# Optimization experiments

Measured on AMD Instinct MI355X. Metric: run time of the kernel, lower is better.

Reference implementation:

```python
import jax, jax.numpy as jnp
import numpy as np

NUM_TAGS = 64
START_TAG = 62
STOP_TAG = 63
NEG = -10000.0
B, L = 512, 512


def setup_inputs() -> dict:
    key = jax.random.key(0)
    k1, k2, k3 = jax.random.split(key, 3)
    inputs = jax.random.normal(k1, (B, L, NUM_TAGS), dtype=jnp.float32)
    tags = jax.random.randint(k2, (B, L), 0, 62)  # real tags only (exclude sentinels)
    mask = jnp.ones((B, L), dtype=jnp.int32)
    transitions = jax.random.normal(k3, (NUM_TAGS, NUM_TAGS), dtype=jnp.float32)
    # match torch __init__: transitions[start_tag, :] = -10000; transitions[:, stop_tag] = -10000
    transitions = transitions.at[START_TAG, :].set(NEG).at[:, STOP_TAG].set(NEG)
    return {"inputs": inputs, "tags": tags, "mask": mask, "transitions": transitions}


def crf_loss(inputs, transitions, tags, mask):
    # inputs: [B, L, T] emissions; transitions[next, prev]; tags/mask: [B, L]
    Bb, Ll, T = inputs.shape
    maskf = mask.astype(inputs.dtype)

    # ---- denominator: forward algorithm (log-sum-exp recurrence over time) ----
    init_alphas = jnp.full((Bb, T), NEG, dtype=inputs.dtype).at[:, START_TAG].set(0.0)

    def step(forward_var, xs):
        emit, m = xs  # emit: [B, T], m: [B]
        # scores[b, next, prev] = fv[b, prev] + (transitions[next, prev] + emit[b, next]) * m[b]
        scores = forward_var[:, None, :] + (transitions[None, :, :] + emit[:, :, None]) * m[:, None, None]
        return jax.nn.logsumexp(scores, axis=-1), None

    forward_var, _ = jax.lax.scan(step, init_alphas, (jnp.swapaxes(inputs, 0, 1), maskf.T))
    terminal = forward_var + transitions[STOP_TAG][None, :]
    log_denominator = jax.nn.logsumexp(terminal, axis=-1)  # [B]

    # ---- numerator: score of the gold tag sequence (fully vectorized over time) ----
    score = transitions[tags[:, 0], START_TAG]  # [B]
    prev_t, next_t = tags[:, :-1], tags[:, 1:]
    trans_sc = transitions[next_t, prev_t]  # [B, L-1]
    emit_sc = jnp.take_along_axis(inputs[:, :-1, :], prev_t[:, :, None], axis=2)[..., 0]  # [B, L-1]
    score = score + jnp.sum(trans_sc * maskf[:, 1:] + emit_sc * maskf[:, :-1], axis=1)
    last_emit = jnp.take_along_axis(inputs[:, -1, :], tags[:, -1:], axis=1)[:, 0]
    score = score + transitions[STOP_TAG, tags[:, -1]] + last_emit * maskf[:, -1]

    return jnp.sum(score - log_denominator)


def reference(inputs, tags, mask, transitions):
    return crf_loss(inputs, transitions, tags, mask)
```

## Files before the change

kernel.cpp:

```cpp
#include <hip/hip_runtime.h>

namespace {

typedef float v2f __attribute__((ext_vector_type(2)));

constexpr int NTAGS = 64;
constexpr int START_T = 62;
constexpr int STOP_T = 63;
constexpr float NEGV = -10000.0f;
constexpr int Bc = 512;
constexpr int Lc = 512;

__device__ __forceinline__ float rfl_f(float v) {
  return __int_as_float(__builtin_amdgcn_readfirstlane(__float_as_int(v)));
}

__device__ __forceinline__ float wave_max(float v) {
#pragma unroll
  for (int off = 32; off >= 1; off >>= 1)
    v = fmaxf(v, __shfl_xor(v, off, 64));
  return v;
}

__device__ __forceinline__ float wave_sum(float v) {
#pragma unroll
  for (int off = 32; off >= 1; off >>= 1)
    v += __shfl_xor(v, off, 64);
  return v;
}

__global__ __launch_bounds__(64, 1) void crf_scan(
    const float* __restrict__ inputs,
    const int* __restrict__ tags,
    const int* __restrict__ mask,
    const float* __restrict__ trans,
    float* __restrict__ partial) {
  __shared__ float4 u4[16];
  float* u1 = reinterpret_cast<float*>(u4);

  const int b = blockIdx.x;
  const int lane = threadIdx.x;

#define FOR16(X) X(0) X(1) X(2) X(3) X(4) X(5) X(6) X(7) \
                 X(8) X(9) X(10) X(11) X(12) X(13) X(14) X(15)

#define DECL_E(q) v2f Ea##q, Eb##q;
  FOR16(DECL_E)
  {
    const float4* row = reinterpret_cast<const float4*>(trans + lane * NTAGS);
#define LOAD_E(q)                                     \
    {                                                 \
      float4 t = row[q];                              \
      Ea##q = (v2f){__expf(t.x), __expf(t.y)};        \
      Eb##q = (v2f){__expf(t.z), __expf(t.w)};        \
    }
    FOR16(LOAD_E)
  }

  const float* emit_base = inputs + (size_t)b * Lc * NTAGS;
  const float* pe = emit_base + lane;
  const int* mask_b = mask + b * Lc;
  const int* tags_b = tags + b * Lc;

  float alpha = (lane == START_T) ? 0.0f : NEGV;
  float m = 0.0f;

#define MF(q, A, B)                                   \
    {                                                 \
      float4 uu = u4[q];                              \
      A += Ea##q * (v2f){uu.x, uu.y};                 \
      B += Eb##q * (v2f){uu.z, uu.w};                 \
    }
#define MS(q)                                         \
    {                                                 \
      float4 uu = u4[q];                              \
      a0 += (v2f){uu.x, uu.y};                        \
      a1 += (v2f){uu.z, uu.w};                        \
    }

#define STEP(EMIT, MIDX)                                              \
    {                                                                 \
      float u_ = __expf(alpha - m);                                   \
      u1[lane] = u_;                                                  \
      __builtin_amdgcn_wave_barrier();                                \
      int mv = __builtin_amdgcn_readlane(mrow, (MIDX));               \
      if (mv) {                                                       \
        v2f a0 = {0.f, 0.f}, a1 = {0.f, 0.f};                         \
        v2f a2 = {0.f, 0.f}, a3 = {0.f, 0.f};                         \
        MF(0, a0, a1) MF(1, a2, a3) MF(2, a0, a1) MF(3, a2, a3)       \
        MF(4, a0, a1) MF(5, a2, a3) MF(6, a0, a1) MF(7, a2, a3)       \
        MF(8, a0, a1) MF(9, a2, a3) MF(10, a0, a1) MF(11, a2, a3)     \
        MF(12, a0, a1) MF(13, a2, a3) MF(14, a0, a1) MF(15, a2, a3)   \
        v2f t = (a0 + a1) + (a2 + a3);                                \
        alpha = __logf(t.x + t.y) + m + (EMIT);                       \
      } else {                                                        \
        v2f a0 = {0.f, 0.f}, a1 = {0.f, 0.f};                         \
        MS(0) MS(1) MS(2) MS(3) MS(4) MS(5) MS(6) MS(7)               \
        MS(8) MS(9) MS(10) MS(11) MS(12) MS(13) MS(14) MS(15)         \
        v2f t = a0 + a1;                                              \
        alpha = __logf(t.x + t.y) + m;                                \
      }                                                               \
      __builtin_amdgcn_wave_barrier();                                \
      m = rfl_f(alpha);                                               \
    }

#define PRE(B0, B1, B2, B3, ST)                                       \
    {                                                                 \
      int s_ = (ST); s_ = s_ > (Lc - 4) ? (Lc - 4) : s_;              \
      B0 = pe[(size_t)(s_ + 0) * NTAGS];                              \
      B1 = pe[(size_t)(s_ + 1) * NTAGS];                              \
      B2 = pe[(size_t)(s_ + 2) * NTAGS];                              \
      B3 = pe[(size_t)(s_ + 3) * NTAGS];                              \
    }

  float eA0, eA1, eA2, eA3, eB0, eB1, eB2, eB3;
  PRE(eA0, eA1, eA2, eA3, 0)
  int mrow = mask_b[lane];

  for (int chunk = 0; chunk < 8; ++chunk) {
    const int cbase = chunk * 64;
    int mrow_nxt = mask_b[(chunk < 7 ? cbase + 64 : cbase) + lane];
    for (int gp = 0; gp < 8; ++gp) {
      const int base = cbase + gp * 8;
      const int mb = gp * 8;
      PRE(eB0, eB1, eB2, eB3, base + 4)
      STEP(eA0, mb + 0) STEP(eA1, mb + 1) STEP(eA2, mb + 2) STEP(eA3, mb + 3)
      PRE(eA0, eA1, eA2, eA3, base + 8)
      STEP(eB0, mb + 4) STEP(eB1, mb + 5) STEP(eB2, mb + 6) STEP(eB3, mb + 7)
    }
    mrow = mrow_nxt;
  }

  float term = alpha + trans[STOP_T * NTAGS + lane];
  float mx = wave_max(term);
  float sden = wave_sum(__expf(term - mx));
  float logden = mx + __logf(sden);

  float sc = 0.0f;
  for (int l = lane; l < Lc; l += 64) {
    int tl = tags_b[l];
    float mfl = (float)mask_b[l];
    if (l < Lc - 1) {
      int tn = tags_b[l + 1];
      float mfn = (float)mask_b[l + 1];
      sc += trans[tn * NTAGS + tl] * mfn +
            emit_base[(size_t)l * NTAGS + tl] * mfl;
    } else {
      sc += trans[STOP_T * NTAGS + tl] +
            emit_base[(size_t)l * NTAGS + tl] * mfl;
    }
  }
  if (lane == 0) sc += trans[tags_b[0] * NTAGS + START_T];
  float score = wave_sum(sc);

  if (lane == 0) partial[b] = score - logden;
}

__global__ void crf_reduce(const float* __restrict__ partial,
                           float* __restrict__ out) {
  const int lane = threadIdx.x;
  float s = 0.0f;
  for (int i = lane; i < Bc; i += 64) s += partial[i];
  s = wave_sum(s);
  if (lane == 0) out[0] = s;
}

}

extern "C" void kernel_launch(void* const* d_in, const int* in_sizes, int n_in,
                              void* d_out, int out_size, void* d_ws,
                              size_t ws_size, hipStream_t stream) {
  const float* inputs = (const float*)d_in[0];
  const int* tags = (const int*)d_in[1];
  const int* mask = (const int*)d_in[2];
  const float* trans = (const float*)d_in[3];
  float* out = (float*)d_out;
  float* partial = (float*)d_ws;

  crf_scan<<<Bc, 64, 0, stream>>>(inputs, tags, mask, trans, partial);
  crf_reduce<<<1, 64, 0, stream>>>(partial, out);
}
```

Baseline: 162.1 us.

## Run CRF forward recurrence in linear space with power-of-two rescaling

Replaces the log-domain forward recurrence with a linear-domain one. Emissions are pre-exponentiated when loaded, and the per-step log/exp pair is removed. Each step rescales the state by a power of two taken from lane 0's exponent bits and keeps a running integer exponent sum, so ln2 is applied only once at the end. This shortens the serial dependency chain per time step, but it risks underflow or overflow when tags differ widely from lane 0 in magnitude.

```diff
diff --git a/kernel.cpp b/kernel.cpp
--- a/kernel.cpp
+++ b/kernel.cpp
@@ -7,13 +7,8 @@
 constexpr int NTAGS = 64;
 constexpr int START_T = 62;
 constexpr int STOP_T = 63;
-constexpr float NEGV = -10000.0f;
 constexpr int Bc = 512;
 constexpr int Lc = 512;
-
-__device__ __forceinline__ float rfl_f(float v) {
-  return __int_as_float(__builtin_amdgcn_readfirstlane(__float_as_int(v)));
-}
 
 __device__ __forceinline__ float wave_max(float v) {
 #pragma unroll
@@ -35,8 +30,8 @@
     const int* __restrict__ mask,
     const float* __restrict__ trans,
     float* __restrict__ partial) {
-  __shared__ float4 u4[16];
-  float* u1 = reinterpret_cast<float*>(u4);
+  __shared__ float4 vb4[16];
+  float* vb1 = reinterpret_cast<float*>(vb4);
 
   const int b = blockIdx.x;
   const int lane = threadIdx.x;
@@ -62,28 +57,27 @@
   const int* mask_b = mask + b * Lc;
   const int* tags_b = tags + b * Lc;
 
-  float alpha = (lane == START_T) ? 0.0f : NEGV;
-  float m = 0.0f;
+  int Msum = 0;
+  vb1[lane] = (lane == START_T) ? 1.0f : 0.0f;
+  __builtin_amdgcn_wave_barrier();
 
-#define MF(q, A, B)                                   \
+#define MF(q, A, Bq)                                  \
     {                                                 \
-      float4 uu = u4[q];                              \
+      float4 uu = vb4[q];                             \
       A += Ea##q * (v2f){uu.x, uu.y};                 \
-      B += Eb##q * (v2f){uu.z, uu.w};                 \
+      Bq += Eb##q * (v2f){uu.z, uu.w};                \
     }
 #define MS(q)                                         \
     {                                                 \
-      float4 uu = u4[q];                              \
+      float4 uu = vb4[q];                             \
       a0 += (v2f){uu.x, uu.y};                        \
       a1 += (v2f){uu.z, uu.w};                        \
     }
 
-#define STEP(EMIT, MIDX)                                              \
+#define STEP(W, MIDX)                                                 \
     {                                                                 \
-      float u_ = __expf(alpha - m);                                   \
-      u1[lane] = u_;                                                  \
-      __builtin_amdgcn_wave_barrier();                                \
-      int mv = __builtin_amdgcn_readlane(mrow, (MIDX));               \
+      const int mv = __builtin_amdgcn_readlane(mrow, (MIDX));         \
+      float s;                                                        \
       if (mv) {                                                       \
         v2f a0 = {0.f, 0.f}, a1 = {0.f, 0.f};                         \
         v2f a2 = {0.f, 0.f}, a3 = {0.f, 0.f};                         \
@@ -92,25 +86,32 @@
         MF(8, a0, a1) MF(9, a2, a3) MF(10, a0, a1) MF(11, a2, a3)     \
         MF(12, a0, a1) MF(13, a2, a3) MF(14, a0, a1) MF(15, a2, a3)   \
         v2f t = (a0 + a1) + (a2 + a3);                                \
-        alpha = __logf(t.x + t.y) + m + (EMIT);                       \
+        s = (t.x + t.y) * (W);                                        \
       } else {                                                        \
         v2f a0 = {0.f, 0.f}, a1 = {0.f, 0.f};                         \
         MS(0) MS(1) MS(2) MS(3) MS(4) MS(5) MS(6) MS(7)               \
         MS(8) MS(9) MS(10) MS(11) MS(12) MS(13) MS(14) MS(15)         \
         v2f t = a0 + a1;                                              \
-        alpha = __logf(t.x + t.y) + m;                                \
+        s = t.x + t.y;                                                \
       }                                                               \
+      const unsigned sb =                                             \
+          (unsigned)__builtin_amdgcn_readfirstlane(__float_as_int(s));\
+      const unsigned e0 = (sb >> 23) & 0xffu;                         \
+      Msum += (int)e0 - 127;                                          \
+      const float r = __uint_as_float((254u - e0) << 23);             \
+      const float vv = s * r;                                         \
       __builtin_amdgcn_wave_barrier();                                \
-      m = rfl_f(alpha);                                               \
+      vb1[lane] = vv;                                                 \
+      __builtin_amdgcn_wave_barrier();                                \
     }
 
 #define PRE(B0, B1, B2, B3, ST)                                       \
     {                                                                 \
       int s_ = (ST); s_ = s_ > (Lc - 4) ? (Lc - 4) : s_;              \
-      B0 = pe[(size_t)(s_ + 0) * NTAGS];                              \
-      B1 = pe[(size_t)(s_ + 1) * NTAGS];                              \
-      B2 = pe[(size_t)(s_ + 2) * NTAGS];                              \
-      B3 = pe[(size_t)(s_ + 3) * NTAGS];                              \
+      B0 = __expf(pe[(size_t)(s_ + 0) * NTAGS]);                      \
+      B1 = __expf(pe[(size_t)(s_ + 1) * NTAGS]);                      \
+      B2 = __expf(pe[(size_t)(s_ + 2) * NTAGS]);                      \
+      B3 = __expf(pe[(size_t)(s_ + 3) * NTAGS]);                      \
     }
 
   float eA0, eA1, eA2, eA3, eB0, eB1, eB2, eB3;
@@ -131,7 +132,11 @@
     mrow = mrow_nxt;
   }
 
-  float term = alpha + trans[STOP_T * NTAGS + lane];
+  const float mf = (float)Msum;
+  const float C = fmaf(mf, -2.1219444e-4f, mf * 0.693359375f);
+
+  float alphav = __logf(vb1[lane]) + C;
+  float term = alphav + trans[STOP_T * NTAGS + lane];
   float mx = wave_max(term);
   float sden = wave_sum(__expf(term - mx));
   float logden = mx + __logf(sden);
```

Result: faster. 152.1 us (-6.2%).

## Interleave two batch rows per wave and scan in linear domain with exponent rescaling

Applied to the files above, without the earlier changes.

Each wave now processes two sequences, alternating their recurrence steps so one chain's LDS round trip and math can overlap the other's. The per-step exp/log of the log-sum-exp is replaced by a linear-domain recurrence. Emissions are exponentiated on prefetch, and scaling uses a power-of-two factor taken from lane 0's float exponent, with the total shift tracked as an integer and converted to log only at the end. Only 256 blocks launch, which halves wave count on a 256-CU part, and the power-of-two rescaling risks underflow or precision loss if values spread widely.

```diff
diff --git a/kernel.cpp b/kernel.cpp
--- a/kernel.cpp
+++ b/kernel.cpp
@@ -7,13 +7,8 @@
 constexpr int NTAGS = 64;
 constexpr int START_T = 62;
 constexpr int STOP_T = 63;
-constexpr float NEGV = -10000.0f;
 constexpr int Bc = 512;
 constexpr int Lc = 512;
-
-__device__ __forceinline__ float rfl_f(float v) {
-  return __int_as_float(__builtin_amdgcn_readfirstlane(__float_as_int(v)));
-}
 
 __device__ __forceinline__ float wave_max(float v) {
 #pragma unroll
@@ -35,11 +30,14 @@
     const int* __restrict__ mask,
     const float* __restrict__ trans,
     float* __restrict__ partial) {
-  __shared__ float4 u4[16];
-  float* u1 = reinterpret_cast<float*>(u4);
-
-  const int b = blockIdx.x;
+  __shared__ float4 bufA[16];
+  __shared__ float4 bufB[16];
+  float* bA1 = reinterpret_cast<float*>(bufA);
+  float* bB1 = reinterpret_cast<float*>(bufB);
+
   const int lane = threadIdx.x;
+  const int bA = blockIdx.x;
+  const int bB = blockIdx.x + 256;
 
 #define FOR16(X) X(0) X(1) X(2) X(3) X(4) X(5) X(6) X(7) \
                  X(8) X(9) X(10) X(11) X(12) X(13) X(14) X(15)
@@ -57,103 +55,155 @@
     FOR16(LOAD_E)
   }
 
-  const float* emit_base = inputs + (size_t)b * Lc * NTAGS;
-  const float* pe = emit_base + lane;
-  const int* mask_b = mask + b * Lc;
-  const int* tags_b = tags + b * Lc;
-
-  float alpha = (lane == START_T) ? 0.0f : NEGV;
-  float m = 0.0f;
-
-#define MF(q, A, B)                                   \
+  const float* embA = inputs + (size_t)bA * Lc * NTAGS;
+  const float* embB = inputs + (size_t)bB * Lc * NTAGS;
+  const float* emA = embA + lane;
+  const float* emB = embB + lane;
+  const int* mAp = mask + bA * Lc;
+  const int* mBp = mask + bB * Lc;
+
+  int MsA = 0, MsB = 0;
+  bA1[lane] = (lane == START_T) ? 1.0f : 0.0f;
+  bB1[lane] = (lane == START_T) ? 1.0f : 0.0f;
+  __builtin_amdgcn_wave_barrier();
+
+  float4 uA[16], uB[16];
+#define ULOAD(U, BUF)                                  \
+  { _Pragma("unroll") for (int q_ = 0; q_ < 16; ++q_) U[q_] = BUF[q_]; }
+
+#define MF(U, q, A, B)                                \
     {                                                 \
-      float4 uu = u4[q];                              \
+      float4 uu = U[q];                               \
       A += Ea##q * (v2f){uu.x, uu.y};                 \
       B += Eb##q * (v2f){uu.z, uu.w};                 \
     }
-#define MS(q)                                         \
+#define MSUM(U, q, A, B)                              \
     {                                                 \
-      float4 uu = u4[q];                              \
-      a0 += (v2f){uu.x, uu.y};                        \
-      a1 += (v2f){uu.z, uu.w};                        \
-    }
-
-#define STEP(EMIT, MIDX)                                              \
-    {                                                                 \
-      float u_ = __expf(alpha - m);                                   \
-      u1[lane] = u_;                                                  \
-      __builtin_amdgcn_wave_barrier();                                \
-      int mv = __builtin_amdgcn_readlane(mrow, (MIDX));               \
-      if (mv) {                                                       \
-        v2f a0 = {0.f, 0.f}, a1 = {0.f, 0.f};                         \
-        v2f a2 = {0.f, 0.f}, a3 = {0.f, 0.f};                         \
-        MF(0, a0, a1) MF(1, a2, a3) MF(2, a0, a1) MF(3, a2, a3)       \
-        MF(4, a0, a1) MF(5, a2, a3) MF(6, a0, a1) MF(7, a2, a3)       \
-        MF(8, a0, a1) MF(9, a2, a3) MF(10, a0, a1) MF(11, a2, a3)     \
-        MF(12, a0, a1) MF(13, a2, a3) MF(14, a0, a1) MF(15, a2, a3)   \
-        v2f t = (a0 + a1) + (a2 + a3);                                \
-        alpha = __logf(t.x + t.y) + m + (EMIT);                       \
-      } else {                                                        \
-        v2f a0 = {0.f, 0.f}, a1 = {0.f, 0.f};                         \
-        MS(0) MS(1) MS(2) MS(3) MS(4) MS(5) MS(6) MS(7)               \
-        MS(8) MS(9) MS(10) MS(11) MS(12) MS(13) MS(14) MS(15)         \
-        v2f t = a0 + a1;                                              \
-        alpha = __logf(t.x + t.y) + m;                                \
-      }                                                               \
-      __builtin_amdgcn_wave_barrier();                                \
-      m = rfl_f(alpha);                                               \
-    }
-
-#define PRE(B0, B1, B2, B3, ST)                                       \
-    {                                                                 \
-      int s_ = (ST); s_ = s_ > (Lc - 4) ? (Lc - 4) : s_;              \
-      B0 = pe[(size_t)(s_ + 0) * NTAGS];                              \
-      B1 = pe[(size_t)(s_ + 1) * NTAGS];                              \
-      B2 = pe[(size_t)(s_ + 2) * NTAGS];                              \
-      B3 = pe[(size_t)(s_ + 3) * NTAGS];                              \
-    }
-
-  float eA0, eA1, eA2, eA3, eB0, eB1, eB2, eB3;
-  PRE(eA0, eA1, eA2, eA3, 0)
-  int mrow = mask_b[lane];
+      float4 uu = U[q];                               \
+      A += (v2f){uu.x, uu.y};                         \
+      B += (v2f){uu.z, uu.w};                         \
+    }
+
+#define COMPUTE(U, W, MROW, MIDX, MS, SOUT)                                 \
+    float SOUT;                                                             \
+    {                                                                       \
+      const int sb_ =                                                       \
+          __builtin_amdgcn_readfirstlane(__float_as_int(U[0].x));           \
+      const unsigned e0_ = ((unsigned)sb_ >> 23) & 0xffu;                   \
+      const int d_ = (e0_ == 0u) ? 0 : (int)e0_ - 127;                      \
+      MS += d_;                                                             \
+      const float rs_ = __uint_as_float((unsigned)(127 - d_) << 23);        \
+      const int mv_ = __builtin_amdgcn_readlane(MROW, (MIDX));              \
+      if (mv_) {                                                            \
+        v2f a0 = {0.f, 0.f}, a1 = {0.f, 0.f};                               \
+        v2f a2 = {0.f, 0.f}, a3 = {0.f, 0.f};                               \
+        MF(U, 0, a0, a1) MF(U, 1, a2, a3) MF(U, 2, a0, a1)                  \
+        MF(U, 3, a2, a3) MF(U, 4, a0, a1) MF(U, 5, a2, a3)                  \
+        MF(U, 6, a0, a1) MF(U, 7, a2, a3) MF(U, 8, a0, a1)                  \
+        MF(U, 9, a2, a3) MF(U, 10, a0, a1) MF(U, 11, a2, a3)                \
+        MF(U, 12, a0, a1) MF(U, 13, a2, a3) MF(U, 14, a0, a1)               \
+        MF(U, 15, a2, a3)                                                   \
+        v2f t_ = (a0 + a1) + (a2 + a3);                                     \
+        SOUT = (t_.x + t_.y) * ((W) * rs_);                                 \
+      } else {                                                              \
+        v2f a0 = {0.f, 0.f}, a1 = {0.f, 0.f};                               \
+        MSUM(U, 0, a0, a1) MSUM(U, 1, a0, a1) MSUM(U, 2, a0, a1)            \
+        MSUM(U, 3, a0, a1) MSUM(U, 4, a0, a1) MSUM(U, 5, a0, a1)            \
+        MSUM(U, 6, a0, a1) MSUM(U, 7, a0, a1) MSUM(U, 8, a0, a1)            \
+        MSUM(U, 9, a0, a1) MSUM(U, 10, a0, a1) MSUM(U, 11, a0, a1)          \
+        MSUM(U, 12, a0, a1) MSUM(U, 13, a0, a1) MSUM(U, 14, a0, a1)         \
+        MSUM(U, 15, a0, a1)                                                 \
+        v2f t_ = a0 + a1;                                                   \
+        SOUT = (t_.x + t_.y) * rs_;                                         \
+      }                                                                     \
+    }
+
+#define ITER(WA_, WB_, MIDX)                           \
+  {                                                    \
+    COMPUTE(uA, WA_, mrA, MIDX, MsA, sA_)              \
+    __builtin_amdgcn_wave_barrier();                   \
+    bA1[lane] = sA_;                                   \
+    __builtin_amdgcn_wave_barrier();                   \
+    ULOAD(uA, bufA)                                    \
+    COMPUTE(uB, WB_, mrB, MIDX, MsB, sB_)              \
+    __builtin_amdgcn_wave_barrier();                   \
+    bB1[lane] = sB_;                                   \
+    __builtin_amdgcn_wave_barrier();                   \
+    ULOAD(uB, bufB)                                    \
+  }
+
+#define PRE(Wb, EM, ST)                                                \
+  {                                                                    \
+    int s_ = (ST); s_ = s_ > (Lc - 4) ? (Lc - 4) : s_;                 \
+    _Pragma("unroll") for (int q_ = 0; q_ < 4; ++q_)                   \
+        Wb[q_] = __expf(EM[(size_t)(s_ + q_) * NTAGS]);                \
+  }
+
+  float wA0[4], wA1v[4], wB0[4], wB1v[4];
+  PRE(wA0, emA, 0)
+  PRE(wB0, emB, 0)
+  int mrA = mAp[lane];
+  int mrB = mBp[lane];
+
+  ULOAD(uA, bufA)
+  ULOAD(uB, bufB)
 
   for (int chunk = 0; chunk < 8; ++chunk) {
     const int cbase = chunk * 64;
-    int mrow_nxt = mask_b[(chunk < 7 ? cbase + 64 : cbase) + lane];
+    const int nb = (chunk < 7 ? cbase + 64 : cbase) + lane;
+    int mrA_nxt = mAp[nb];
+    int mrB_nxt = mBp[nb];
     for (int gp = 0; gp < 8; ++gp) {
       const int base = cbase + gp * 8;
       const int mb = gp * 8;
-      PRE(eB0, eB1, eB2, eB3, base + 4)
-      STEP(eA0, mb + 0) STEP(eA1, mb + 1) STEP(eA2, mb + 2) STEP(eA3, mb + 3)
-      PRE(eA0, eA1, eA2, eA3, base + 8)
-      STEP(eB0, mb + 4) STEP(eB1, mb + 5) STEP(eB2, mb + 6) STEP(eB3, mb + 7)
-    }
-    mrow = mrow_nxt;
-  }
-
-  float term = alpha + trans[STOP_T * NTAGS + lane];
-  float mx = wave_max(term);
-  float sden = wave_sum(__expf(term - mx));
-  float logden = mx + __logf(sden);
-
-  float sc = 0.0f;
-  for (int l = lane; l < Lc; l += 64) {
-    int tl = tags_b[l];
-    float mfl = (float)mask_b[l];
-    if (l < Lc - 1) {
-      int tn = tags_b[l + 1];
-      float mfn = (float)mask_b[l + 1];
-      sc += trans[tn * NTAGS + tl] * mfn +
-            emit_base[(size_t)l * NTAGS + tl] * mfl;
-    } else {
-      sc += trans[STOP_T * NTAGS + tl] +
-            emit_base[(size_t)l * NTAGS + tl] * mfl;
-    }
-  }
-  if (lane == 0) sc += trans[tags_b[0] * NTAGS + START_T];
-  float score = wave_sum(sc);
-
-  if (lane == 0) partial[b] = score - logden;
+      PRE(wA1v, emA, base + 4)
+      PRE(wB1v, emB, base + 4)
+      ITER(wA0[0], wB0[0], mb + 0)
+      ITER(wA0[1], wB0[1], mb + 1)
+      ITER(wA0[2], wB0[2], mb + 2)
+      ITER(wA0[3], wB0[3], mb + 3)
+      PRE(wA0, emA, base + 8)
+      PRE(wB0, emB, base + 8)
+      ITER(wA1v[0], wB1v[0], mb + 4)
+      ITER(wA1v[1], wB1v[1], mb + 5)
+      ITER(wA1v[2], wB1v[2], mb + 6)
+      ITER(wA1v[3], wB1v[3], mb + 7)
+    }
+    mrA = mrA_nxt;
+    mrB = mrB_nxt;
+  }
+
+#define EPILOGUE(BUF1, MS, EMB, BIDX, MP)                              \
+  {                                                                    \
+    const float mf_ = (float)(MS);                                     \
+    const float C_ = fmaf(mf_, -2.1219444e-4f, mf_ * 0.693359375f);    \
+    float alphav = __logf(BUF1[lane]) + C_;                            \
+    float term = alphav + trans[STOP_T * NTAGS + lane];                \
+    float mx = wave_max(term);                                         \
+    float sden = wave_sum(__expf(term - mx));                          \
+    float logden = mx + __logf(sden);                                  \
+    const int* tb_ = tags + (BIDX) * Lc;                               \
+    float sc = 0.0f;                                                   \
+    for (int l = lane; l < Lc; l += 64) {                              \
+      int tl = tb_[l];                                                 \
+      float mfl = (float)MP[l];                                        \
+      if (l < Lc - 1) {                                                \
+        int tn = tb_[l + 1];                                           \
+        float mfn = (float)MP[l + 1];                                  \
+        sc += trans[tn * NTAGS + tl] * mfn +                           \
+              (EMB)[(size_t)l * NTAGS + tl] * mfl;                     \
+      } else {                                                         \
+        sc += trans[STOP_T * NTAGS + tl] +                             \
+              (EMB)[(size_t)l * NTAGS + tl] * mfl;                     \
+      }                                                                \
+    }                                                                  \
+    if (lane == 0) sc += trans[tb_[0] * NTAGS + START_T];              \
+    float score = wave_sum(sc);                                        \
+    if (lane == 0) partial[BIDX] = score - logden;                     \
+  }
+
+  EPILOGUE(bA1, MsA, embA, bA, mAp)
+  EPILOGUE(bB1, MsB, embB, bB, mBp)
 }
 
 __global__ void crf_reduce(const float* __restrict__ partial,
@@ -177,6 +227,6 @@
   float* out = (float*)d_out;
   float* partial = (float*)d_ws;
 
-  crf_scan<<<Bc, 64, 0, stream>>>(inputs, tags, mask, trans, partial);
+  crf_scan<<<Bc / 2, 64, 0, stream>>>(inputs, tags, mask, trans, partial);
   crf_reduce<<<1, 64, 0, stream>>>(partial, out);
 }
```

New measurement: 204.1 us. +25.9%, slower.
